# Optimization experiments

Hardware: AMD Instinct MI355X
Metric: run time of the kernel (lower is better)

Reference implementation:

```python
import jax, jax.numpy as jnp
import numpy as np

B, T, D = 4, 4096, 768
N = 256           # events per doc
HID = 200


def setup_inputs() -> dict:
    key = jax.random.key(0)
    k = jax.random.split(key, 8)
    event_embed = jax.random.normal(k[0], (B, T, D), dtype=jnp.float32)
    event_idx = jax.random.randint(k[1], (B, N), 0, T)
    W1 = jax.random.normal(k[2], (3 * D, HID), dtype=jnp.float32) * 0.02
    b1 = jnp.zeros((HID,), jnp.float32)
    W2 = jax.random.normal(k[3], (HID, HID), dtype=jnp.float32) * 0.02
    b2 = jnp.zeros((HID,), jnp.float32)
    W3 = jax.random.normal(k[4], (HID, 1), dtype=jnp.float32) * 0.02
    b3 = jnp.zeros((1,), jnp.float32)
    return {"event_embed": event_embed, "event_idx": event_idx,
            "W1": W1, "b1": b1, "W2": W2, "b2": b2, "W3": W3, "b3": b3}


def reference(event_embed, event_idx, W1, b1, W2, b2, W3, b3):
    n = event_idx.shape[1]
    # gather event embeddings: [B, N, D]
    emb = jnp.take_along_axis(event_embed, event_idx[..., None], axis=1)
    # all ordered pairs (i, j) with j < i (antecedents)
    ii, jj = jnp.tril_indices(n, k=-1)          # each [P], P = N(N-1)/2
    i_g = emb[:, ii, :]                          # [B, P, D]
    j_g = emb[:, jj, :]
    pairs = jnp.concatenate((i_g, j_g, i_g * j_g), axis=-1)   # [B, P, 3D]
    # 3-layer MLP score (dropout is identity in eval mode)
    h = jax.nn.relu(jnp.einsum('bpe,eh->bph', pairs, W1) + b1)
    h = jax.nn.relu(jnp.einsum('bph,hk->bpk', h, W2) + b2)
    s = (jnp.einsum('bph,ho->bpo', h, W3) + b3)[..., 0]        # [B, P]
    # scatter into score matrix; diagonal = epsilon score 0.0
    S = jnp.zeros((emb.shape[0], n, n), dtype=s.dtype)
    S = S.at[:, ii, jj].set(s)
    valid = (jnp.arange(n)[None, :] <= jnp.arange(n)[:, None])  # j <= i
    logits = jnp.where(valid[None], S, -jnp.inf)
    probs = jax.nn.softmax(logits, axis=-1)                    # row-wise softmax
    return jnp.where(valid[None], probs, jnp.float32(-1000.0))  # pad value -1000
```

## Files before the change

### kernel.cpp

```cpp
#include <hip/hip_runtime.h>


#define NB 4
#define NN 256
#define DD 768
#define TT 4096
#define HP 224
#define NTILES 14
#define KT1 24
#define KT2 7
#define TRI 136
#define ABS 448
#define MTS 3584

typedef _Float16 f16x8 __attribute__((ext_vector_type(8)));
typedef _Float16 f16x2 __attribute__((ext_vector_type(2)));
typedef __attribute__((ext_vector_type(4))) float f32x4;

union FragU { uint4 u; f16x8 h; };
union H2U { unsigned int u; f16x2 h; };

__device__ __forceinline__ unsigned int h2mul(unsigned int a, unsigned int b) {
    H2U x, y, r; x.u = a; y.u = b; r.h = x.h * y.h;
    return r.u;
}
__device__ __forceinline__ float hlo(unsigned int v) { H2U x; x.u = v; return (float)x.h[0]; }
__device__ __forceinline__ float hhi(unsigned int v) { H2U x; x.u = v; return (float)x.h[1]; }
__device__ __forceinline__ unsigned short f2h(float f) {
    _Float16 h = (_Float16)f;
    union { _Float16 h; unsigned short u; } r; r.h = h; return r.u;
}
__device__ __forceinline__ float h2f(unsigned short u) {
    union { unsigned short u; _Float16 h; } r; r.u = u; return (float)r.h;
}

__global__ void prep_all(const float* __restrict__ W1, const float* __restrict__ W2,
                         const float* __restrict__ ee, const int* __restrict__ eidx,
                         unsigned short* __restrict__ w1n,
                         unsigned short* __restrict__ w1s,
                         unsigned short* __restrict__ w2s,
                         unsigned short* __restrict__ emb) {
    const int N1n = 24 * 28 * 512;
    const int N1s = 24 * 14 * 512;
    const int N2  = 7 * 14 * 512;
    int bx = blockIdx.x;
    if (bx >= 2212) {
        int g = bx - 2212;
        int b = g >> 8, n = g & 255;
        int t = eidx[b * NN + n];
        const float* src = ee + ((size_t)b * TT + t) * DD;
        unsigned short* dst = emb + ((size_t)b * NN + n) * DD;
        for (int e = threadIdx.x; e < DD; e += 256) dst[e] = f2h(src[e]);
        return;
    }
    int idx = bx * 256 + threadIdx.x;
    if (idx < N1n) {
        int j = idx & 7, lane = (idx >> 3) & 63, f = idx >> 9;
        int nt = f % 28, kt = f / 28;
        int k = kt * 32 + (lane >> 4) * 8 + j;
        int n = nt * 16 + (lane & 15);
        float v;
        if (n < HP) v = (n < 200) ? W1[(size_t)k * 200 + n] : 0.f;
        else { int c2 = n - HP; v = (c2 < 200) ? W1[(size_t)(768 + k) * 200 + c2] : 0.f; }
        w1n[idx] = f2h(v);
    } else if (idx < N1n + N1s) {
        int i2 = idx - N1n;
        int j = i2 & 7, lane = (i2 >> 3) & 63, f = i2 >> 9;
        int nt = f % NTILES, kt = f / NTILES;
        int k = kt * 32 + (lane >> 4) * 8 + j;
        int n = nt * 16 + (lane & 15);
        float v = (n < 200) ? W1[(size_t)(1536 + k) * 200 + n] : 0.f;
        w1s[i2] = f2h(v);
    } else if (idx < N1n + N1s + N2) {
        int i2 = idx - N1n - N1s;
        int j = i2 & 7, lane = (i2 >> 3) & 63, f = i2 >> 9;
        int nt = f % NTILES, kt = f / NTILES;
        int k = kt * 32 + (lane >> 4) * 8 + j;
        int n = nt * 16 + (lane & 15);
        float v = (k < 200 && n < 200) ? W2[(size_t)k * 200 + n] : 0.f;
        w2s[i2] = f2h(v);
    }
}

__global__ __launch_bounds__(64)
void node_mfma(const unsigned short* __restrict__ emb,
               const unsigned short* __restrict__ w1n,
               unsigned short* __restrict__ AB) {
    int lane = threadIdx.x & 63;
    int q = lane >> 4, c = lane & 15;
    int mt = blockIdx.x >> 2;
    int ng = blockIdx.x & 3;
    int m0 = mt * 16;
    const uint4* ga = (const uint4*)emb + (size_t)(m0 + c) * 96;
    const uint4* gb = (const uint4*)w1n;

    f32x4 acc[7];
#pragma unroll
    for (int n = 0; n < 7; ++n) acc[n] = (f32x4){0.f, 0.f, 0.f, 0.f};

    uint4 aA, aB, bA[7], bB[7];
    aA = ga[q];
#pragma unroll
    for (int n = 0; n < 7; ++n) bA[n] = gb[((0 * 28 + ng * 7 + n) << 6) + lane];

#pragma unroll 1
    for (int kt = 0; kt < KT1; kt += 2) {
        aB = ga[(kt + 1) * 4 + q];
#pragma unroll
        for (int n = 0; n < 7; ++n) bB[n] = gb[(((kt + 1) * 28 + ng * 7 + n) << 6) + lane];
        {
            FragU a; a.u = aA;
#pragma unroll
            for (int n = 0; n < 7; ++n) {
                FragU bb; bb.u = bA[n];
                acc[n] = __builtin_amdgcn_mfma_f32_16x16x32_f16(a.h, bb.h, acc[n], 0, 0, 0);
            }
        }
        if (kt + 2 < KT1) {
            aA = ga[(kt + 2) * 4 + q];
#pragma unroll
            for (int n = 0; n < 7; ++n) bA[n] = gb[(((kt + 2) * 28 + ng * 7 + n) << 6) + lane];
        }
        {
            FragU a; a.u = aB;
#pragma unroll
            for (int n = 0; n < 7; ++n) {
                FragU bb; bb.u = bB[n];
                acc[n] = __builtin_amdgcn_mfma_f32_16x16x32_f16(a.h, bb.h, acc[n], 0, 0, 0);
            }
        }
    }
#pragma unroll
    for (int n = 0; n < 7; ++n) {
        int col = (ng * 7 + n) * 16 + c;
#pragma unroll
        for (int rr = 0; rr < 4; ++rr)
            AB[(size_t)(m0 + q * 4 + rr) * ABS + col] = f2h(acc[n][rr]);
    }
}

__global__ __launch_bounds__(128, 3)
void pair_wave(
    const unsigned short* __restrict__ emb,
    const unsigned short* __restrict__ w1s,
    const unsigned short* __restrict__ w2s,
    const unsigned short* __restrict__ AB,
    const float* __restrict__ b1, const float* __restrict__ b2,
    const float* __restrict__ W3, const float* __restrict__ b3,
    float* __restrict__ S) {
    int bid = blockIdx.x;
    int rp = bid / 544;
    int g = bid % 544;
    int b = g / TRI;
    int r = g % TRI;
    int ti = (int)((sqrtf(8.f * (float)r + 1.f) - 1.f) * 0.5f);
    while ((ti + 1) * (ti + 2) / 2 <= r) ++ti;
    while (ti * (ti + 1) / 2 > r) --ti;
    int tj = r - ti * (ti + 1) / 2;
    int i0 = ti << 4, j0 = tj << 4;

    int tid = threadIdx.x;
    int lane = tid & 63;
    int nh = tid >> 6;
    int q = lane >> 4, c = lane & 15;
    int iA = i0 + rp * 2, iB = iA + 1;

    __shared__ __align__(16) unsigned short smH[2 * MTS];
    __shared__ float sred[2][32];
    unsigned short* slot0 = smH;
    unsigned short* slot1 = smH + MTS;

    const uint4* w1f = (const uint4*)w1s;
    const uint4* w2f = (const uint4*)w2s;
    const uint4* gI0 = (const uint4*)(emb + ((size_t)b * NN + iA) * DD);
    const uint4* gI1 = (const uint4*)(emb + ((size_t)b * NN + iB) * DD);
    const uint4* gJc = (const uint4*)(emb + ((size_t)b * NN + j0 + c) * DD);

    f32x4 acc[2][7];
#pragma unroll
    for (int t = 0; t < 2; ++t)
#pragma unroll
        for (int n = 0; n < 7; ++n)
            acc[t][n] = (f32x4){0.f, 0.f, 0.f, 0.f};

    {
        uint4 bfrA[7], bfrB[7];
        uint4 ejA, e0A, e1A, ejB, e0B, e1B;
#pragma unroll
        for (int n = 0; n < 7; ++n) bfrA[n] = w1f[(nh * 7 + n) * 64 + lane];
        ejA = gJc[q]; e0A = gI0[q]; e1A = gI1[q];

#pragma unroll 1
        for (int kt = 0; kt < KT1; kt += 2) {
#pragma unroll
            for (int n = 0; n < 7; ++n)
                bfrB[n] = w1f[((kt + 1) * NTILES + nh * 7 + n) * 64 + lane];
            ejB = gJc[(kt + 1) * 4 + q]; e0B = gI0[(kt + 1) * 4 + q]; e1B = gI1[(kt + 1) * 4 + q];
            {
                FragU a0, a1;
                a0.u.x = h2mul(e0A.x, ejA.x); a0.u.y = h2mul(e0A.y, ejA.y);
                a0.u.z = h2mul(e0A.z, ejA.z); a0.u.w = h2mul(e0A.w, ejA.w);
                a1.u.x = h2mul(e1A.x, ejA.x); a1.u.y = h2mul(e1A.y, ejA.y);
                a1.u.z = h2mul(e1A.z, ejA.z); a1.u.w = h2mul(e1A.w, ejA.w);
#pragma unroll
                for (int n = 0; n < 7; ++n) {
                    FragU bb; bb.u = bfrA[n];
                    acc[0][n] = __builtin_amdgcn_mfma_f32_16x16x32_f16(a0.h, bb.h, acc[0][n], 0, 0, 0);
                    acc[1][n] = __builtin_amdgcn_mfma_f32_16x16x32_f16(a1.h, bb.h, acc[1][n], 0, 0, 0);
                }
            }
            if (kt + 2 < KT1) {
#pragma unroll
                for (int n = 0; n < 7; ++n)
                    bfrA[n] = w1f[((kt + 2) * NTILES + nh * 7 + n) * 64 + lane];
                ejA = gJc[(kt + 2) * 4 + q]; e0A = gI0[(kt + 2) * 4 + q]; e1A = gI1[(kt + 2) * 4 + q];
            }
            {
                FragU a0, a1;
                a0.u.x = h2mul(e0B.x, ejB.x); a0.u.y = h2mul(e0B.y, ejB.y);
                a0.u.z = h2mul(e0B.z, ejB.z); a0.u.w = h2mul(e0B.w, ejB.w);
                a1.u.x = h2mul(e1B.x, ejB.x); a1.u.y = h2mul(e1B.y, ejB.y);
                a1.u.z = h2mul(e1B.z, ejB.z); a1.u.w = h2mul(e1B.w, ejB.w);
#pragma unroll
                for (int n = 0; n < 7; ++n) {
                    FragU bb; bb.u = bfrB[n];
                    acc[0][n] = __builtin_amdgcn_mfma_f32_16x16x32_f16(a0.h, bb.h, acc[0][n], 0, 0, 0);
                    acc[1][n] = __builtin_amdgcn_mfma_f32_16x16x32_f16(a1.h, bb.h, acc[1][n], 0, 0, 0);
                }
            }
        }
    }

    {
        float af0[7], af1[7];
        unsigned int bvp[7][2];
#pragma unroll
        for (int n = 0; n < 7; ++n) {
            int h = ((nh * 7 + n) << 4) + c;
            float b1v = (h < 200) ? b1[h] : 0.f;
            af0[n] = h2f(AB[((size_t)b * NN + iA) * ABS + h]) + b1v;
            af1[n] = h2f(AB[((size_t)b * NN + iB) * ABS + h]) + b1v;
#pragma unroll
            for (int p = 0; p < 2; ++p) {
                unsigned int lo = AB[((size_t)b * NN + j0 + q * 4 + 2 * p) * ABS + HP + h];
                unsigned int hi = AB[((size_t)b * NN + j0 + q * 4 + 2 * p + 1) * ABS + HP + h];
                bvp[n][p] = (hi << 16) | lo;
            }
        }
#pragma unroll
        for (int n = 0; n < 7; ++n) {
            int h = ((nh * 7 + n) << 4) + c;
            int kk2 = h >> 5, q2 = (h >> 3) & 3, j2 = h & 7;
            int fa = ((kk2 * 4 + q2) << 7) + j2;
#pragma unroll
            for (int rr = 0; rr < 4; ++rr) {
                float bvf = (rr & 1) ? hhi(bvp[n][rr >> 1]) : hlo(bvp[n][rr >> 1]);
                int ad = fa + ((q * 4 + rr) << 3);
                slot0[ad] = f2h(fmaxf(acc[0][n][rr] + af0[n] + bvf, 0.f));
                slot1[ad] = f2h(fmaxf(acc[1][n][rr] + af1[n] + bvf, 0.f));
            }
        }
    }
    __syncthreads();

    f32x4 acc2[2][7];
#pragma unroll
    for (int t = 0; t < 2; ++t)
#pragma unroll
        for (int n = 0; n < 7; ++n)
            acc2[t][n] = (f32x4){0.f, 0.f, 0.f, 0.f};

    {
        uint4 bfrA[7], bfrB[7];
#pragma unroll
        for (int n = 0; n < 7; ++n) bfrA[n] = w2f[(nh * 7 + n) * 64 + lane];

#pragma unroll 1
        for (int kk = 0; kk < 6; kk += 2) {
#pragma unroll
            for (int n = 0; n < 7; ++n)
                bfrB[n] = w2f[((kk + 1) * NTILES + nh * 7 + n) * 64 + lane];
            {
                FragU a20, a21;
                a20.u = *(const uint4*)(&slot0[(((kk * 4 + q) * 16 + c) << 3)]);
                a21.u = *(const uint4*)(&slot1[(((kk * 4 + q) * 16 + c) << 3)]);
#pragma unroll
                for (int n = 0; n < 7; ++n) {
                    FragU bb; bb.u = bfrA[n];
                    acc2[0][n] = __builtin_amdgcn_mfma_f32_16x16x32_f16(a20.h, bb.h, acc2[0][n], 0, 0, 0);
                    acc2[1][n] = __builtin_amdgcn_mfma_f32_16x16x32_f16(a21.h, bb.h, acc2[1][n], 0, 0, 0);
                }
            }
#pragma unroll
            for (int n = 0; n < 7; ++n)
                bfrA[n] = w2f[((kk + 2) * NTILES + nh * 7 + n) * 64 + lane];
            {
                FragU a20, a21;
                a20.u = *(const uint4*)(&slot0[((((kk + 1) * 4 + q) * 16 + c) << 3)]);
                a21.u = *(const uint4*)(&slot1[((((kk + 1) * 4 + q) * 16 + c) << 3)]);
#pragma unroll
                for (int n = 0; n < 7; ++n) {
                    FragU bb; bb.u = bfrB[n];
                    acc2[0][n] = __builtin_amdgcn_mfma_f32_16x16x32_f16(a20.h, bb.h, acc2[0][n], 0, 0, 0);
                    acc2[1][n] = __builtin_amdgcn_mfma_f32_16x16x32_f16(a21.h, bb.h, acc2[1][n], 0, 0, 0);
                }
            }
        }
        {
            FragU a20, a21;
            a20.u = *(const uint4*)(&slot0[(((6 * 4 + q) * 16 + c) << 3)]);
            a21.u = *(const uint4*)(&slot1[(((6 * 4 + q) * 16 + c) << 3)]);
#pragma unroll
            for (int n = 0; n < 7; ++n) {
                FragU bb; bb.u = bfrA[n];
                acc2[0][n] = __builtin_amdgcn_mfma_f32_16x16x32_f16(a20.h, bb.h, acc2[0][n], 0, 0, 0);
                acc2[1][n] = __builtin_amdgcn_mfma_f32_16x16x32_f16(a21.h, bb.h, acc2[1][n], 0, 0, 0);
            }
        }
    }

    {
        float b2v[7], w3v[7];
#pragma unroll
        for (int n = 0; n < 7; ++n) {
            int h = ((nh * 7 + n) << 4) + c;
            b2v[n] = (h < 200) ? b2[h] : 0.f;
            w3v[n] = (h < 200) ? W3[h] : 0.f;
        }
#pragma unroll
        for (int t = 0; t < 2; ++t) {
#pragma unroll
            for (int rr = 0; rr < 4; ++rr) {
                float part = 0.f;
#pragma unroll
                for (int n = 0; n < 7; ++n) {
                    float hv = fmaxf(acc2[t][n][rr] + b2v[n], 0.f);
                    part += hv * w3v[n];
                }
                part += __shfl_xor(part, 1);
                part += __shfl_xor(part, 2);
                part += __shfl_xor(part, 4);
                part += __shfl_xor(part, 8);
                if (c == 0)
                    sred[nh][t * 16 + q * 4 + rr] = part;
            }
        }
    }
    __syncthreads();

    if (tid < 32) {
        int t = tid >> 4, jj = tid & 15;
        float s = sred[0][tid] + sred[1][tid] + b3[0];
        S[((size_t)b * NN + iA + t) * NN + j0 + jj] = s;
    }
}

__global__ __launch_bounds__(256) void softmax_rows(const float* __restrict__ S,
                                                    float* __restrict__ out) {
    int b = blockIdx.x >> 8, i = blockIdx.x & 255;
    int j = threadIdx.x;
    int lane = j & 63, w = j >> 6;
    __shared__ float red[16];
    float x = (j < i) ? S[((size_t)b * NN + i) * NN + j] : ((j == i) ? 0.f : -1e30f);
    float m = x;
#pragma unroll
    for (int off = 32; off; off >>= 1) m = fmaxf(m, __shfl_xor(m, off));
    if (lane == 0) red[w] = m;
    __syncthreads();
    float mx = fmaxf(fmaxf(red[0], red[1]), fmaxf(red[2], red[3]));
    float e = (j <= i) ? __expf(x - mx) : 0.f;
    float s = e;
#pragma unroll
    for (int off = 32; off; off >>= 1) s += __shfl_xor(s, off);
    if (lane == 0) red[8 + w] = s;
    __syncthreads();
    float sum = red[8] + red[9] + red[10] + red[11];
    out[((size_t)b * NN + i) * NN + j] = (j <= i) ? (e / sum) : -1000.0f;
}

extern "C" void kernel_launch(void* const* d_in, const int* in_sizes, int n_in,
                              void* d_out, int out_size, void* d_ws, size_t ws_size,
                              hipStream_t stream) {
    const float* ee  = (const float*)d_in[0];
    const int*   eidx = (const int*)d_in[1];
    const float* W1  = (const float*)d_in[2];
    const float* b1  = (const float*)d_in[3];
    const float* W2  = (const float*)d_in[4];
    const float* b2  = (const float*)d_in[5];
    const float* W3  = (const float*)d_in[6];
    const float* b3  = (const float*)d_in[7];
    float* out = (float*)d_out;

    char* p = (char*)d_ws;
    unsigned short* emb = (unsigned short*)p; p += (size_t)NB * NN * DD * 2;
    unsigned short* w1n = (unsigned short*)p; p += (size_t)24 * 28 * 512 * 2;
    unsigned short* w1s = (unsigned short*)p; p += (size_t)24 * 14 * 512 * 2;
    unsigned short* w2s = (unsigned short*)p; p += (size_t)7 * 14 * 512 * 2;
    unsigned short* AB  = (unsigned short*)p; p += (size_t)NB * NN * ABS * 2;
    float* S  = (float*)p; p += (size_t)NB * NN * NN * 4;

    prep_all<<<3236, 256, 0, stream>>>(W1, W2, ee, eidx, w1n, w1s, w2s, emb);
    node_mfma<<<256, 64, 0, stream>>>(emb, w1n, AB);
    pair_wave<<<4352, 128, 0, stream>>>(emb, w1s, w2s, AB, b1, b2, W3, b3, S);
    softmax_rows<<<NB * NN, 256, 0, stream>>>(S, out);
}
```

Baseline: 215.6 us.

## Process four anchor rows per pair block to reuse weight fragments

Each pair_wave block now computes four i-rows of a 16-wide j tile instead of two, so every W1 and W2 fragment loaded from global memory feeds four MFMA chains instead of two. The grid is halved and LDS grows to hold four hidden-activation slots. Launch bounds drop from 3 to 2 blocks per CU to make room for the doubled accumulator registers. The trade-off is fewer resident waves for latency hiding and more register pressure, in exchange for half the weight traffic per pair.

```diff
diff --git a/kernel.cpp b/kernel.cpp
--- a/kernel.cpp
+++ b/kernel.cpp
@@ -139,7 +139,7 @@
     }
 }
 
-__global__ __launch_bounds__(128, 3)
+__global__ __launch_bounds__(128, 2)
 void pair_wave(
     const unsigned short* __restrict__ emb,
     const unsigned short* __restrict__ w1s,
@@ -163,83 +163,81 @@
     int lane = tid & 63;
     int nh = tid >> 6;
     int q = lane >> 4, c = lane & 15;
-    int iA = i0 + rp * 2, iB = iA + 1;
-
-    __shared__ __align__(16) unsigned short smH[2 * MTS];
-    __shared__ float sred[2][32];
-    unsigned short* slot0 = smH;
-    unsigned short* slot1 = smH + MTS;
+    int iA = i0 + rp * 4;
+
+    __shared__ __align__(16) unsigned short smH[4 * MTS];
+    __shared__ float sred[2][64];
 
     const uint4* w1f = (const uint4*)w1s;
     const uint4* w2f = (const uint4*)w2s;
-    const uint4* gI0 = (const uint4*)(emb + ((size_t)b * NN + iA) * DD);
-    const uint4* gI1 = (const uint4*)(emb + ((size_t)b * NN + iB) * DD);
+    const uint4* gI[4];
+#pragma unroll
+    for (int t = 0; t < 4; ++t)
+        gI[t] = (const uint4*)(emb + ((size_t)b * NN + iA + t) * DD);
     const uint4* gJc = (const uint4*)(emb + ((size_t)b * NN + j0 + c) * DD);
 
-    f32x4 acc[2][7];
-#pragma unroll
-    for (int t = 0; t < 2; ++t)
+    f32x4 acc[4][7];
+#pragma unroll
+    for (int t = 0; t < 4; ++t)
 #pragma unroll
         for (int n = 0; n < 7; ++n)
             acc[t][n] = (f32x4){0.f, 0.f, 0.f, 0.f};
 
     {
         uint4 bfrA[7], bfrB[7];
-        uint4 ejA, e0A, e1A, ejB, e0B, e1B;
+        uint4 ejA, ejB, eA[4], eB[4];
 #pragma unroll
         for (int n = 0; n < 7; ++n) bfrA[n] = w1f[(nh * 7 + n) * 64 + lane];
-        ejA = gJc[q]; e0A = gI0[q]; e1A = gI1[q];
+        ejA = gJc[q];
+#pragma unroll
+        for (int t = 0; t < 4; ++t) eA[t] = gI[t][q];
 
 #pragma unroll 1
         for (int kt = 0; kt < KT1; kt += 2) {
 #pragma unroll
             for (int n = 0; n < 7; ++n)
                 bfrB[n] = w1f[((kt + 1) * NTILES + nh * 7 + n) * 64 + lane];
-            ejB = gJc[(kt + 1) * 4 + q]; e0B = gI0[(kt + 1) * 4 + q]; e1B = gI1[(kt + 1) * 4 + q];
-            {
-                FragU a0, a1;
-                a0.u.x = h2mul(e0A.x, ejA.x); a0.u.y = h2mul(e0A.y, ejA.y);
-                a0.u.z = h2mul(e0A.z, ejA.z); a0.u.w = h2mul(e0A.w, ejA.w);
-                a1.u.x = h2mul(e1A.x, ejA.x); a1.u.y = h2mul(e1A.y, ejA.y);
-                a1.u.z = h2mul(e1A.z, ejA.z); a1.u.w = h2mul(e1A.w, ejA.w);
+            ejB = gJc[(kt + 1) * 4 + q];
+#pragma unroll
+            for (int t = 0; t < 4; ++t) eB[t] = gI[t][(kt + 1) * 4 + q];
+#pragma unroll
+            for (int t = 0; t < 4; ++t) {
+                FragU a;
+                a.u.x = h2mul(eA[t].x, ejA.x); a.u.y = h2mul(eA[t].y, ejA.y);
+                a.u.z = h2mul(eA[t].z, ejA.z); a.u.w = h2mul(eA[t].w, ejA.w);
 #pragma unroll
                 for (int n = 0; n < 7; ++n) {
                     FragU bb; bb.u = bfrA[n];
-                    acc[0][n] = __builtin_amdgcn_mfma_f32_16x16x32_f16(a0.h, bb.h, acc[0][n], 0, 0, 0);
-                    acc[1][n] = __builtin_amdgcn_mfma_f32_16x16x32_f16(a1.h, bb.h, acc[1][n], 0, 0, 0);
+                    acc[t][n] = __builtin_amdgcn_mfma_f32_16x16x32_f16(a.h, bb.h, acc[t][n], 0, 0, 0);
                 }
             }
             if (kt + 2 < KT1) {
 #pragma unroll
                 for (int n = 0; n < 7; ++n)
                     bfrA[n] = w1f[((kt + 2) * NTILES + nh * 7 + n) * 64 + lane];
-                ejA = gJc[(kt + 2) * 4 + q]; e0A = gI0[(kt + 2) * 4 + q]; e1A = gI1[(kt + 2) * 4 + q];
-            }
-            {
-                FragU a0, a1;
-                a0.u.x = h2mul(e0B.x, ejB.x); a0.u.y = h2mul(e0B.y, ejB.y);
-                a0.u.z = h2mul(e0B.z, ejB.z); a0.u.w = h2mul(e0B.w, ejB.w);
-                a1.u.x = h2mul(e1B.x, ejB.x); a1.u.y = h2mul(e1B.y, ejB.y);
-                a1.u.z = h2mul(e1B.z, ejB.z); a1.u.w = h2mul(e1B.w, ejB.w);
+                ejA = gJc[(kt + 2) * 4 + q];
+#pragma unroll
+                for (int t = 0; t < 4; ++t) eA[t] = gI[t][(kt + 2) * 4 + q];
+            }
+#pragma unroll
+            for (int t = 0; t < 4; ++t) {
+                FragU a;
+                a.u.x = h2mul(eB[t].x, ejB.x); a.u.y = h2mul(eB[t].y, ejB.y);
+                a.u.z = h2mul(eB[t].z, ejB.z); a.u.w = h2mul(eB[t].w, ejB.w);
 #pragma unroll
                 for (int n = 0; n < 7; ++n) {
                     FragU bb; bb.u = bfrB[n];
-                    acc[0][n] = __builtin_amdgcn_mfma_f32_16x16x32_f16(a0.h, bb.h, acc[0][n], 0, 0, 0);
-                    acc[1][n] = __builtin_amdgcn_mfma_f32_16x16x32_f16(a1.h, bb.h, acc[1][n], 0, 0, 0);
+                    acc[t][n] = __builtin_amdgcn_mfma_f32_16x16x32_f16(a.h, bb.h, acc[t][n], 0, 0, 0);
                 }
             }
         }
     }
 
     {
-        float af0[7], af1[7];
         unsigned int bvp[7][2];
 #pragma unroll
         for (int n = 0; n < 7; ++n) {
             int h = ((nh * 7 + n) << 4) + c;
-            float b1v = (h < 200) ? b1[h] : 0.f;
-            af0[n] = h2f(AB[((size_t)b * NN + iA) * ABS + h]) + b1v;
-            af1[n] = h2f(AB[((size_t)b * NN + iB) * ABS + h]) + b1v;
 #pragma unroll
             for (int p = 0; p < 2; ++p) {
                 unsigned int lo = AB[((size_t)b * NN + j0 + q * 4 + 2 * p) * ABS + HP + h];
@@ -248,24 +246,29 @@
             }
         }
 #pragma unroll
-        for (int n = 0; n < 7; ++n) {
-            int h = ((nh * 7 + n) << 4) + c;
-            int kk2 = h >> 5, q2 = (h >> 3) & 3, j2 = h & 7;
-            int fa = ((kk2 * 4 + q2) << 7) + j2;
-#pragma unroll
-            for (int rr = 0; rr < 4; ++rr) {
-                float bvf = (rr & 1) ? hhi(bvp[n][rr >> 1]) : hlo(bvp[n][rr >> 1]);
-                int ad = fa + ((q * 4 + rr) << 3);
-                slot0[ad] = f2h(fmaxf(acc[0][n][rr] + af0[n] + bvf, 0.f));
-                slot1[ad] = f2h(fmaxf(acc[1][n][rr] + af1[n] + bvf, 0.f));
+        for (int t = 0; t < 4; ++t) {
+            unsigned short* slot = &smH[t * MTS];
+#pragma unroll
+            for (int n = 0; n < 7; ++n) {
+                int h = ((nh * 7 + n) << 4) + c;
+                float b1v = (h < 200) ? b1[h] : 0.f;
+                float af = h2f(AB[((size_t)b * NN + iA + t) * ABS + h]) + b1v;
+                int kk2 = h >> 5, q2 = (h >> 3) & 3, j2 = h & 7;
+                int fa = ((kk2 * 4 + q2) << 7) + j2;
+#pragma unroll
+                for (int rr = 0; rr < 4; ++rr) {
+                    float bvf = (rr & 1) ? hhi(bvp[n][rr >> 1]) : hlo(bvp[n][rr >> 1]);
+                    slot[fa + ((q * 4 + rr) << 3)] =
+                        f2h(fmaxf(acc[t][n][rr] + af + bvf, 0.f));
+                }
             }
         }
     }
     __syncthreads();
 
-    f32x4 acc2[2][7];
-#pragma unroll
-    for (int t = 0; t < 2; ++t)
+    f32x4 acc2[4][7];
+#pragma unroll
+    for (int t = 0; t < 4; ++t)
 #pragma unroll
         for (int n = 0; n < 7; ++n)
             acc2[t][n] = (f32x4){0.f, 0.f, 0.f, 0.f};
@@ -280,41 +283,38 @@
 #pragma unroll
             for (int n = 0; n < 7; ++n)
                 bfrB[n] = w2f[((kk + 1) * NTILES + nh * 7 + n) * 64 + lane];
-            {
-                FragU a20, a21;
-                a20.u = *(const uint4*)(&slot0[(((kk * 4 + q) * 16 + c) << 3)]);
-                a21.u = *(const uint4*)(&slot1[(((kk * 4 + q) * 16 + c) << 3)]);
+#pragma unroll
+            for (int t = 0; t < 4; ++t) {
+                FragU a2;
+                a2.u = *(const uint4*)(&smH[t * MTS + (((kk * 4 + q) * 16 + c) << 3)]);
 #pragma unroll
                 for (int n = 0; n < 7; ++n) {
                     FragU bb; bb.u = bfrA[n];
-                    acc2[0][n] = __builtin_amdgcn_mfma_f32_16x16x32_f16(a20.h, bb.h, acc2[0][n], 0, 0, 0);
-                    acc2[1][n] = __builtin_amdgcn_mfma_f32_16x16x32_f16(a21.h, bb.h, acc2[1][n], 0, 0, 0);
+                    acc2[t][n] = __builtin_amdgcn_mfma_f32_16x16x32_f16(a2.h, bb.h, acc2[t][n], 0, 0, 0);
                 }
             }
 #pragma unroll
             for (int n = 0; n < 7; ++n)
                 bfrA[n] = w2f[((kk + 2) * NTILES + nh * 7 + n) * 64 + lane];
-            {
-                FragU a20, a21;
-                a20.u = *(const uint4*)(&slot0[((((kk + 1) * 4 + q) * 16 + c) << 3)]);
-                a21.u = *(const uint4*)(&slot1[((((kk + 1) * 4 + q) * 16 + c) << 3)]);
+#pragma unroll
+            for (int t = 0; t < 4; ++t) {
+                FragU a2;
+                a2.u = *(const uint4*)(&smH[t * MTS + ((((kk + 1) * 4 + q) * 16 + c) << 3)]);
 #pragma unroll
                 for (int n = 0; n < 7; ++n) {
                     FragU bb; bb.u = bfrB[n];
-                    acc2[0][n] = __builtin_amdgcn_mfma_f32_16x16x32_f16(a20.h, bb.h, acc2[0][n], 0, 0, 0);
-                    acc2[1][n] = __builtin_amdgcn_mfma_f32_16x16x32_f16(a21.h, bb.h, acc2[1][n], 0, 0, 0);
-                }
-            }
-        }
-        {
-            FragU a20, a21;
-            a20.u = *(const uint4*)(&slot0[(((6 * 4 + q) * 16 + c) << 3)]);
-            a21.u = *(const uint4*)(&slot1[(((6 * 4 + q) * 16 + c) << 3)]);
+                    acc2[t][n] = __builtin_amdgcn_mfma_f32_16x16x32_f16(a2.h, bb.h, acc2[t][n], 0, 0, 0);
+                }
+            }
+        }
+#pragma unroll
+        for (int t = 0; t < 4; ++t) {
+            FragU a2;
+            a2.u = *(const uint4*)(&smH[t * MTS + (((6 * 4 + q) * 16 + c) << 3)]);
 #pragma unroll
             for (int n = 0; n < 7; ++n) {
                 FragU bb; bb.u = bfrA[n];
-                acc2[0][n] = __builtin_amdgcn_mfma_f32_16x16x32_f16(a20.h, bb.h, acc2[0][n], 0, 0, 0);
-                acc2[1][n] = __builtin_amdgcn_mfma_f32_16x16x32_f16(a21.h, bb.h, acc2[1][n], 0, 0, 0);
+                acc2[t][n] = __builtin_amdgcn_mfma_f32_16x16x32_f16(a2.h, bb.h, acc2[t][n], 0, 0, 0);
             }
         }
     }
@@ -328,7 +328,7 @@
             w3v[n] = (h < 200) ? W3[h] : 0.f;
         }
 #pragma unroll
-        for (int t = 0; t < 2; ++t) {
+        for (int t = 0; t < 4; ++t) {
 #pragma unroll
             for (int rr = 0; rr < 4; ++rr) {
                 float part = 0.f;
@@ -348,7 +348,7 @@
     }
     __syncthreads();
 
-    if (tid < 32) {
+    if (tid < 64) {
         int t = tid >> 4, jj = tid & 15;
         float s = sred[0][tid] + sred[1][tid] + b3[0];
         S[((size_t)b * NN + iA + t) * NN + j0 + jj] = s;
@@ -401,6 +401,6 @@
 
     prep_all<<<3236, 256, 0, stream>>>(W1, W2, ee, eidx, w1n, w1s, w2s, emb);
     node_mfma<<<256, 64, 0, stream>>>(emb, w1n, AB);
-    pair_wave<<<4352, 128, 0, stream>>>(emb, w1s, w2s, AB, b1, b2, W3, b3, S);
+    pair_wave<<<2176, 128, 0, stream>>>(emb, w1s, w2s, AB, b1, b2, W3, b3, S);
     softmax_rows<<<NB * NN, 256, 0, stream>>>(S, out);
 }
```

New measurement: 209.3 us. -2.9%, faster.
